# Optimization experiments

Hardware: AMD Instinct MI355X
Metric: run time of the kernel (lower is better)

The kernel has to match this reference:

```python
import jax, jax.numpy as jnp
import numpy as np

N, D, C, P = 4096, 512, 100, 64
EPS_COS = 1e-8   # torch cosine_similarity norm clamp
EPS_INV = 1e-5   # module's 1/(d + 1e-5)


def setup_inputs() -> dict:
    key = jax.random.key(0)
    k1, k2, k3, k4 = jax.random.split(key, 4)
    feats = jax.random.normal(k1, (N, D), dtype=jnp.float32)
    protos = jax.random.normal(k2, (C, P, D), dtype=jnp.float32)
    cls_ids = jax.random.randint(k3, (N,), 0, C)
    proto_labels = jax.random.randint(k4, (C, P), 0, 1000)
    return {"feats": feats, "protos": protos, "cls_ids": cls_ids,
            "proto_labels": proto_labels}


def reference(feats, protos, cls_ids, proto_labels):
    # Gather each box's class-conditional prototype set: [N, P, D]
    p = protos[cls_ids]
    pl = proto_labels[cls_ids]                       # [N, P]

    # cosine distance: 1 - f.p / (max(|f|,eps) * max(|p|,eps))
    dot = jnp.einsum('nd,npd->np', feats, p)         # [N, P]
    fnorm = jnp.maximum(jnp.linalg.norm(feats, axis=-1, keepdims=True), EPS_COS)
    pnorm = jnp.maximum(jnp.linalg.norm(p, axis=-1), EPS_COS)
    d_cos = 1.0 - dot / (fnorm * pnorm)

    diff = feats[:, None, :] - p                     # [N, P, D]
    d_l1 = jnp.mean(jnp.abs(diff), axis=-1)          # F.l1_loss (mean)
    d_l2 = jnp.mean(diff * diff, axis=-1)            # F.mse_loss (mean)

    dists = jnp.stack([d_cos, d_l1, d_l2], axis=1)   # [N, 3, P]
    probs = jax.nn.softmax(1.0 / (dists + EPS_INV), axis=-1).mean(axis=1)  # [N, P]

    idx = jnp.argmax(probs, axis=-1)                 # [N]
    labels = jnp.take_along_axis(pl, idx[:, None], axis=1)[:, 0]
    return labels, probs
```

## Files before the change

kernel.cpp:

```cpp
#include <hip/hip_runtime.h>

#define D 512
#define P 64
#define CHUNK 16
#define MAXD 1152
#define EPS_COS 1e-8f
#define EPS_INV 1e-5f


__device__ __forceinline__ float wave_sum(float v) {
#pragma unroll
    for (int m = 32; m >= 1; m >>= 1) v += __shfl_xor(v, m, 64);
    return v;
}

__global__ __launch_bounds__(256) void proto_norm_kernel(
    const float* __restrict__ protos, float* __restrict__ pp, int rows)
{
    const int lane = threadIdx.x & 63;
    const int r = blockIdx.x * 4 + (threadIdx.x >> 6);
    if (r >= rows) return;
    const float* row = protos + (size_t)r * D;
    const float4 a = *(const float4*)(row + lane * 4);
    const float4 b = *(const float4*)(row + 256 + lane * 4);
    float s = a.x*a.x + a.y*a.y + a.z*a.z + a.w*a.w
            + b.x*b.x + b.y*b.y + b.z*b.z + b.w*b.w;
    s = wave_sum(s);
    if (lane == 0) pp[r] = s;
}

__global__ __launch_bounds__(1024) void setup_kernel(
    const int* __restrict__ cls, int* __restrict__ sorted,
    int* __restrict__ desc, int N, int C)
{
    __shared__ int cnt[128], fl[128], exc[128], arr[128];
    const int t = threadIdx.x;
    if (t < 128) { cnt[t] = 0; fl[t] = 0; arr[t] = 0; }
    for (int i = t; i < 3 * MAXD; i += 1024) desc[i] = 0;
    __syncthreads();
#pragma unroll
    for (int k = 0; k < 4; ++k) {
        const int n = t + 1024 * k;
        if (n < N) atomicAdd(&cnt[cls[n]], 1);
    }
    __syncthreads();
    int v = 0, gv = 0, pos = 0;
    if (t < 128) {
        v = cnt[t];
        gv = (v + CHUNK - 1) / CHUNK;
        pos = ((t & 3) << 5) | (t >> 2);
        exc[t] = v;
        arr[pos] = gv;
    }
    __syncthreads();
    for (int d = 1; d < 128; d <<= 1) {
        int a = 0, b = 0;
        if (t < 128 && t >= d) { a = exc[t - d]; b = arr[t - d]; }
        __syncthreads();
        if (t < 128 && t >= d) { exc[t] += a; arr[t] += b; }
        __syncthreads();
    }
    int base = 0;
    if (t < 128) base = exc[t] - v;
    __syncthreads();
    if (t < 128) exc[t] = base;
    __syncthreads();
    if (t < C && gv > 0) {
        const int b = t & 3;
        const int bstart = (pos >= 32) ? arr[(pos & ~31) - 1] : 0;
        const int localoff = (arr[pos] - gv) - bstart;
        for (int k = 0; k < gv; ++k) {
            const int slot = ((localoff + k) << 2) | b;
            desc[3*slot+0] = t;
            desc[3*slot+1] = base + CHUNK * k;
            desc[3*slot+2] = min(CHUNK, v - CHUNK * k);
        }
    }
#pragma unroll
    for (int k = 0; k < 4; ++k) {
        const int n = t + 1024 * k;
        if (n < N) {
            const int c = cls[n];
            const int p2 = exc[c] + atomicAdd(&fl[c], 1);
            sorted[p2] = n;
        }
    }
}

__global__ __launch_bounds__(256, 3) void proto_dist_kernel(
    const float* __restrict__ feats,
    const float* __restrict__ protos,
    const int*   __restrict__ sorted,
    const int*   __restrict__ desc,
    float* __restrict__ dist)
{
    const int di   = blockIdx.x >> 1;
    const int half = blockIdx.x & 1;
    const int cnt  = desc[3*di+2];
    if (cnt == 0) return;
    const int cls   = desc[3*di+0];
    const int start = desc[3*di+1];
    const int lane = threadIdx.x & 63;
    const int wave = threadIdx.x >> 6;

    int  nidx[4];
    bool valid[4];
#pragma unroll
    for (int k = 0; k < 4; ++k) {
        const int pos = wave + 4 * k;
        valid[k] = pos < cnt;
        nidx[k]  = sorted[start + (valid[k] ? pos : (cnt - 1))];
    }

    float4 f0[4], f1[4];
#pragma unroll
    for (int b = 0; b < 4; ++b) {
        const float* f = feats + (size_t)nidx[b] * D;
        f0[b] = *(const float4*)(f + lane * 4);
        f1[b] = *(const float4*)(f + 256 + lane * 4);
    }

    const float* pr = protos + (size_t)cls * (P * D) + (size_t)half * (32 * D);
    const bool hi32 = (lane & 32) != 0;
    const bool hi16 = (lane & 16) != 0;
    const bool hi8  = (lane & 8)  != 0;

    float r_dot[4], r_l1[4];

    for (int g = 0; g < 4; ++g) {
        float pd[4][8], pl[4][8];
#pragma unroll
        for (int j = 0; j < 8; ++j) {
            const float* row = pr + (size_t)(8 * g + j) * D;
            const float4 q0 = *(const float4*)(row + lane * 4);
            const float4 q1 = *(const float4*)(row + 256 + lane * 4);
#pragma unroll
            for (int b = 0; b < 4; ++b) {
                float dot, l1, t;
                dot  = f0[b].x*q0.x; t = f0[b].x - q0.x; l1  = fabsf(t);
                dot += f0[b].y*q0.y; t = f0[b].y - q0.y; l1 += fabsf(t);
                dot += f0[b].z*q0.z; t = f0[b].z - q0.z; l1 += fabsf(t);
                dot += f0[b].w*q0.w; t = f0[b].w - q0.w; l1 += fabsf(t);
                dot += f1[b].x*q1.x; t = f1[b].x - q1.x; l1 += fabsf(t);
                dot += f1[b].y*q1.y; t = f1[b].y - q1.y; l1 += fabsf(t);
                dot += f1[b].z*q1.z; t = f1[b].z - q1.z; l1 += fabsf(t);
                dot += f1[b].w*q1.w; t = f1[b].w - q1.w; l1 += fabsf(t);
                pd[b][j] = dot; pl[b][j] = l1;
            }
        }
#pragma unroll
        for (int b = 0; b < 4; ++b) {
#pragma unroll
            for (int k = 0; k < 4; ++k) {
                const float sd = hi32 ? pd[b][k] : pd[b][k+4];
                const float sl = hi32 ? pl[b][k] : pl[b][k+4];
                const float rd = __shfl_xor(sd, 32, 64);
                const float rl = __shfl_xor(sl, 32, 64);
                pd[b][k] = (hi32 ? pd[b][k+4] : pd[b][k]) + rd;
                pl[b][k] = (hi32 ? pl[b][k+4] : pl[b][k]) + rl;
            }
#pragma unroll
            for (int k = 0; k < 2; ++k) {
                const float sd = hi16 ? pd[b][k] : pd[b][k+2];
                const float sl = hi16 ? pl[b][k] : pl[b][k+2];
                const float rd = __shfl_xor(sd, 16, 64);
                const float rl = __shfl_xor(sl, 16, 64);
                pd[b][k] = (hi16 ? pd[b][k+2] : pd[b][k]) + rd;
                pl[b][k] = (hi16 ? pl[b][k+2] : pl[b][k]) + rl;
            }
            {
                const float sd = hi8 ? pd[b][0] : pd[b][1];
                const float sl = hi8 ? pl[b][0] : pl[b][1];
                const float rd = __shfl_xor(sd, 8, 64);
                const float rl = __shfl_xor(sl, 8, 64);
                pd[b][0] = (hi8 ? pd[b][1] : pd[b][0]) + rd;
                pl[b][0] = (hi8 ? pl[b][1] : pl[b][0]) + rl;
            }
#pragma unroll
            for (int m = 4; m >= 1; m >>= 1) {
                pd[b][0] += __shfl_xor(pd[b][0], m, 64);
                pl[b][0] += __shfl_xor(pl[b][0], m, 64);
            }
            if ((lane & 3) == g) { r_dot[b] = pd[b][0]; r_l1[b] = pl[b][0]; }
        }
    }

    const int pg   = 32 * half + 8 * (lane & 3) + ((lane >> 3) & 7);
    const int qsel = (lane >> 2) & 1;
#pragma unroll
    for (int k = 0; k < 4; ++k) {
        if (valid[k]) {
            dist[((size_t)nidx[k] * P + pg) * 2 + qsel] = qsel ? r_l1[k] : r_dot[k];
        }
    }
}

__global__ __launch_bounds__(256) void softmax_kernel(
    const float* __restrict__ feats,
    const int*   __restrict__ cls_ids,
    const int*   __restrict__ proto_labels,
    const float* __restrict__ ppbuf,
    const float* __restrict__ dist,
    float* __restrict__ out, int N)
{
    const int lane = threadIdx.x & 63;
    const int n = blockIdx.x * 4 + (threadIdx.x >> 6);
    if (n >= N) return;
    const int cls = cls_ids[n];

    const float* f = feats + (size_t)n * D;
    const float4 a = *(const float4*)(f + lane * 4);
    const float4 b = *(const float4*)(f + 256 + lane * 4);
    float ffv = a.x*a.x + a.y*a.y + a.z*a.z + a.w*a.w
              + b.x*b.x + b.y*b.y + b.z*b.z + b.w*b.w;
    ffv = wave_sum(ffv);

    const float2 dl = *(const float2*)&dist[((size_t)n * P + lane) * 2];
    const float ppv   = ppbuf[cls * P + lane];
    const float fnorm = fmaxf(sqrtf(ffv), EPS_COS);
    const float pnorm = fmaxf(sqrtf(ppv), EPS_COS);
    const float d_cos = 1.0f - dl.x / (fnorm * pnorm);
    const float d_l1  = dl.y * (1.0f / (float)D);
    const float d_l2  = (ffv - 2.0f * dl.x + ppv) * (1.0f / (float)D);

    float sc[3];
    sc[0] = 1.0f / (d_cos + EPS_INV);
    sc[1] = 1.0f / (d_l1  + EPS_INV);
    sc[2] = 1.0f / (d_l2  + EPS_INV);

    float prob = 0.f;
#pragma unroll
    for (int i = 0; i < 3; ++i) {
        float m = sc[i];
#pragma unroll
        for (int w = 32; w >= 1; w >>= 1) m = fmaxf(m, __shfl_xor(m, w, 64));
        const float e = expf(sc[i] - m);
        prob += e / wave_sum(e);
    }
    prob *= (1.0f / 3.0f);

    float best = prob;
    int   bidx = lane;
#pragma unroll
    for (int w = 32; w >= 1; w >>= 1) {
        const float ov = __shfl_xor(best, w, 64);
        const int   oi = __shfl_xor(bidx, w, 64);
        if (ov > best || (ov == best && oi < bidx)) { best = ov; bidx = oi; }
    }

    out[(size_t)N + (size_t)n * P + lane] = prob;
    if (lane == 0) out[n] = (float)proto_labels[cls * P + bidx];
}

extern "C" void kernel_launch(void* const* d_in, const int* in_sizes, int n_in,
                              void* d_out, int out_size, void* d_ws, size_t ws_size,
                              hipStream_t stream) {
    const float* feats        = (const float*)d_in[0];
    const float* protos       = (const float*)d_in[1];
    const int*   cls_ids      = (const int*)d_in[2];
    const int*   proto_labels = (const int*)d_in[3];
    float* out = (float*)d_out;

    const int N    = in_sizes[2];
    const int rows = in_sizes[1] / D;
    const int C    = rows / P;

    char* w = (char*)d_ws;
    float* pp     = (float*)w;
    int*   sorted = (int*)(w + 25600);
    int*   desc   = (int*)(w + 41984);
    float* dist   = (float*)(w + 57344);

    proto_norm_kernel<<<(rows + 3) / 4, 256, 0, stream>>>(protos, pp, rows);
    setup_kernel<<<1, 1024, 0, stream>>>(cls_ids, sorted, desc, N, C);
    proto_dist_kernel<<<2 * MAXD, 256, 0, stream>>>(feats, protos, sorted, desc, dist);
    softmax_kernel<<<(N + 3) / 4, 256, 0, stream>>>(
        feats, cls_ids, proto_labels, pp, dist, out, N);
}
```

Baseline: 119.8 us.

## Fuse softmax into distance kernel and merge prep kernels into one launch

Merges the prototype-norm and class-sorting setup into one prep kernel, where block 0 does the sort and the other blocks compute norms. The distance and softmax stages become one kernel that handles all 64 prototypes per block for chunks of 4 features, computes feature norms inline, and writes probabilities and labels directly. This removes two launches and the intermediate distance buffer round trip through global memory. In exchange, each prototype set is re-read for fewer features, so L2 traffic on prototypes grows. Descriptor slots are now bounds-checked against the enlarged table.

```diff
diff --git a/kernel.cpp b/kernel.cpp
--- a/kernel.cpp
+++ b/kernel.cpp
@@ -2,8 +2,8 @@
 
 #define D 512
 #define P 64
-#define CHUNK 16
-#define MAXD 1152
+#define CHUNK 4
+#define MAXD 1536
 #define EPS_COS 1e-8f
 #define EPS_INV 1e-5f
 
@@ -14,33 +14,33 @@
     return v;
 }
 
-__global__ __launch_bounds__(256) void proto_norm_kernel(
-    const float* __restrict__ protos, float* __restrict__ pp, int rows)
+__global__ __launch_bounds__(256) void prep_kernel(
+    const float* __restrict__ protos, const int* __restrict__ cls,
+    float* __restrict__ pp, int* __restrict__ sorted, int* __restrict__ desc,
+    int N, int C, int rows)
 {
-    const int lane = threadIdx.x & 63;
-    const int r = blockIdx.x * 4 + (threadIdx.x >> 6);
-    if (r >= rows) return;
-    const float* row = protos + (size_t)r * D;
-    const float4 a = *(const float4*)(row + lane * 4);
-    const float4 b = *(const float4*)(row + 256 + lane * 4);
-    float s = a.x*a.x + a.y*a.y + a.z*a.z + a.w*a.w
-            + b.x*b.x + b.y*b.y + b.z*b.z + b.w*b.w;
-    s = wave_sum(s);
-    if (lane == 0) pp[r] = s;
-}
-
-__global__ __launch_bounds__(1024) void setup_kernel(
-    const int* __restrict__ cls, int* __restrict__ sorted,
-    int* __restrict__ desc, int N, int C)
-{
+    if (blockIdx.x != 0) {
+        const int lane = threadIdx.x & 63;
+        const int r = (blockIdx.x - 1) * 4 + (threadIdx.x >> 6);
+        if (r >= rows) return;
+        const float* row = protos + (size_t)r * D;
+        const float4 a = *(const float4*)(row + lane * 4);
+        const float4 b = *(const float4*)(row + 256 + lane * 4);
+        float s = a.x*a.x + a.y*a.y + a.z*a.z + a.w*a.w
+                + b.x*b.x + b.y*b.y + b.z*b.z + b.w*b.w;
+        s = wave_sum(s);
+        if (lane == 0) pp[r] = s;
+        return;
+    }
+
     __shared__ int cnt[128], fl[128], exc[128], arr[128];
     const int t = threadIdx.x;
     if (t < 128) { cnt[t] = 0; fl[t] = 0; arr[t] = 0; }
-    for (int i = t; i < 3 * MAXD; i += 1024) desc[i] = 0;
-    __syncthreads();
-#pragma unroll
-    for (int k = 0; k < 4; ++k) {
-        const int n = t + 1024 * k;
+    for (int i = t; i < 3 * MAXD; i += 256) desc[i] = 0;
+    __syncthreads();
+#pragma unroll
+    for (int k = 0; k < 16; ++k) {
+        const int n = t + 256 * k;
         if (n < N) atomicAdd(&cnt[cls[n]], 1);
     }
     __syncthreads();
@@ -48,7 +48,7 @@
     if (t < 128) {
         v = cnt[t];
         gv = (v + CHUNK - 1) / CHUNK;
-        pos = ((t & 3) << 5) | (t >> 2);
+        pos = ((t & 7) << 4) | (t >> 3);
         exc[t] = v;
         arr[pos] = gv;
     }
@@ -60,25 +60,26 @@
         if (t < 128 && t >= d) { exc[t] += a; arr[t] += b; }
         __syncthreads();
     }
-    int base = 0;
-    if (t < 128) base = exc[t] - v;
+    const int base = (t < 128) ? exc[t] - v : 0;
     __syncthreads();
     if (t < 128) exc[t] = base;
     __syncthreads();
     if (t < C && gv > 0) {
-        const int b = t & 3;
-        const int bstart = (pos >= 32) ? arr[(pos & ~31) - 1] : 0;
+        const int bucket = t & 7;
+        const int bstart = bucket ? arr[(bucket << 4) - 1] : 0;
         const int localoff = (arr[pos] - gv) - bstart;
         for (int k = 0; k < gv; ++k) {
-            const int slot = ((localoff + k) << 2) | b;
-            desc[3*slot+0] = t;
-            desc[3*slot+1] = base + CHUNK * k;
-            desc[3*slot+2] = min(CHUNK, v - CHUNK * k);
-        }
-    }
-#pragma unroll
-    for (int k = 0; k < 4; ++k) {
-        const int n = t + 1024 * k;
+            const int slot = ((localoff + k) << 3) | bucket;
+            if (slot < MAXD) {
+                desc[3*slot+0] = t;
+                desc[3*slot+1] = base + CHUNK * k;
+                desc[3*slot+2] = min(CHUNK, v - CHUNK * k);
+            }
+        }
+    }
+#pragma unroll
+    for (int k = 0; k < 16; ++k) {
+        const int n = t + 256 * k;
         if (n < N) {
             const int c = cls[n];
             const int p2 = exc[c] + atomicAdd(&fl[c], 1);
@@ -87,55 +88,62 @@
     }
 }
 
-__global__ __launch_bounds__(256, 3) void proto_dist_kernel(
+__global__ __launch_bounds__(128) void proto_main_kernel(
     const float* __restrict__ feats,
     const float* __restrict__ protos,
+    const int*   __restrict__ proto_labels,
+    const float* __restrict__ ppbuf,
     const int*   __restrict__ sorted,
     const int*   __restrict__ desc,
-    float* __restrict__ dist)
+    float* __restrict__ out, int N)
 {
-    const int di   = blockIdx.x >> 1;
-    const int half = blockIdx.x & 1;
-    const int cnt  = desc[3*di+2];
+    const int di  = blockIdx.x;
+    const int cnt = desc[3*di+2];
     if (cnt == 0) return;
     const int cls   = desc[3*di+0];
     const int start = desc[3*di+1];
     const int lane = threadIdx.x & 63;
     const int wave = threadIdx.x >> 6;
 
-    int  nidx[4];
-    bool valid[4];
-#pragma unroll
-    for (int k = 0; k < 4; ++k) {
-        const int pos = wave + 4 * k;
+    int  nidx[2];
+    bool valid[2];
+#pragma unroll
+    for (int k = 0; k < 2; ++k) {
+        const int pos = wave + 2 * k;
         valid[k] = pos < cnt;
         nidx[k]  = sorted[start + (valid[k] ? pos : (cnt - 1))];
     }
 
-    float4 f0[4], f1[4];
-#pragma unroll
-    for (int b = 0; b < 4; ++b) {
+    float4 f0[2], f1[2];
+    float  ff[2];
+#pragma unroll
+    for (int b = 0; b < 2; ++b) {
         const float* f = feats + (size_t)nidx[b] * D;
         f0[b] = *(const float4*)(f + lane * 4);
         f1[b] = *(const float4*)(f + 256 + lane * 4);
-    }
-
-    const float* pr = protos + (size_t)cls * (P * D) + (size_t)half * (32 * D);
+        float s = f0[b].x*f0[b].x + f0[b].y*f0[b].y + f0[b].z*f0[b].z + f0[b].w*f0[b].w
+                + f1[b].x*f1[b].x + f1[b].y*f1[b].y + f1[b].z*f1[b].z + f1[b].w*f1[b].w;
+        ff[b] = wave_sum(s);
+    }
+
+    const float* pr = protos + (size_t)cls * (P * D);
+    const int jsel = (lane >> 3) & 7;
+    const int gown = lane & 7;
     const bool hi32 = (lane & 32) != 0;
     const bool hi16 = (lane & 16) != 0;
     const bool hi8  = (lane & 8)  != 0;
 
-    float r_dot[4], r_l1[4];
-
-    for (int g = 0; g < 4; ++g) {
-        float pd[4][8], pl[4][8];
+    float r_dot[2] = {0.f, 0.f}, r_l1[2] = {0.f, 0.f};
+
+    for (int g = 0; g < 8; ++g) {
+        float pd[2][8], pl[2][8];
 #pragma unroll
         for (int j = 0; j < 8; ++j) {
             const float* row = pr + (size_t)(8 * g + j) * D;
             const float4 q0 = *(const float4*)(row + lane * 4);
             const float4 q1 = *(const float4*)(row + 256 + lane * 4);
 #pragma unroll
-            for (int b = 0; b < 4; ++b) {
+            for (int b = 0; b < 2; ++b) {
                 float dot, l1, t;
                 dot  = f0[b].x*q0.x; t = f0[b].x - q0.x; l1  = fabsf(t);
                 dot += f0[b].y*q0.y; t = f0[b].y - q0.y; l1 += fabsf(t);
@@ -149,7 +157,7 @@
             }
         }
 #pragma unroll
-        for (int b = 0; b < 4; ++b) {
+        for (int b = 0; b < 2; ++b) {
 #pragma unroll
             for (int k = 0; k < 4; ++k) {
                 const float sd = hi32 ? pd[b][k] : pd[b][k+4];
@@ -181,75 +189,51 @@
                 pd[b][0] += __shfl_xor(pd[b][0], m, 64);
                 pl[b][0] += __shfl_xor(pl[b][0], m, 64);
             }
-            if ((lane & 3) == g) { r_dot[b] = pd[b][0]; r_l1[b] = pl[b][0]; }
-        }
-    }
-
-    const int pg   = 32 * half + 8 * (lane & 3) + ((lane >> 3) & 7);
-    const int qsel = (lane >> 2) & 1;
-#pragma unroll
-    for (int k = 0; k < 4; ++k) {
-        if (valid[k]) {
-            dist[((size_t)nidx[k] * P + pg) * 2 + qsel] = qsel ? r_l1[k] : r_dot[k];
-        }
-    }
-}
-
-__global__ __launch_bounds__(256) void softmax_kernel(
-    const float* __restrict__ feats,
-    const int*   __restrict__ cls_ids,
-    const int*   __restrict__ proto_labels,
-    const float* __restrict__ ppbuf,
-    const float* __restrict__ dist,
-    float* __restrict__ out, int N)
-{
-    const int lane = threadIdx.x & 63;
-    const int n = blockIdx.x * 4 + (threadIdx.x >> 6);
-    if (n >= N) return;
-    const int cls = cls_ids[n];
-
-    const float* f = feats + (size_t)n * D;
-    const float4 a = *(const float4*)(f + lane * 4);
-    const float4 b = *(const float4*)(f + 256 + lane * 4);
-    float ffv = a.x*a.x + a.y*a.y + a.z*a.z + a.w*a.w
-              + b.x*b.x + b.y*b.y + b.z*b.z + b.w*b.w;
-    ffv = wave_sum(ffv);
-
-    const float2 dl = *(const float2*)&dist[((size_t)n * P + lane) * 2];
-    const float ppv   = ppbuf[cls * P + lane];
-    const float fnorm = fmaxf(sqrtf(ffv), EPS_COS);
-    const float pnorm = fmaxf(sqrtf(ppv), EPS_COS);
-    const float d_cos = 1.0f - dl.x / (fnorm * pnorm);
-    const float d_l1  = dl.y * (1.0f / (float)D);
-    const float d_l2  = (ffv - 2.0f * dl.x + ppv) * (1.0f / (float)D);
-
-    float sc[3];
-    sc[0] = 1.0f / (d_cos + EPS_INV);
-    sc[1] = 1.0f / (d_l1  + EPS_INV);
-    sc[2] = 1.0f / (d_l2  + EPS_INV);
-
-    float prob = 0.f;
-#pragma unroll
-    for (int i = 0; i < 3; ++i) {
-        float m = sc[i];
-#pragma unroll
-        for (int w = 32; w >= 1; w >>= 1) m = fmaxf(m, __shfl_xor(m, w, 64));
-        const float e = expf(sc[i] - m);
-        prob += e / wave_sum(e);
-    }
-    prob *= (1.0f / 3.0f);
-
-    float best = prob;
-    int   bidx = lane;
-#pragma unroll
-    for (int w = 32; w >= 1; w >>= 1) {
-        const float ov = __shfl_xor(best, w, 64);
-        const int   oi = __shfl_xor(bidx, w, 64);
-        if (ov > best || (ov == best && oi < bidx)) { best = ov; bidx = oi; }
-    }
-
-    out[(size_t)N + (size_t)n * P + lane] = prob;
-    if (lane == 0) out[n] = (float)proto_labels[cls * P + bidx];
+            if (gown == g) { r_dot[b] = pd[b][0]; r_l1[b] = pl[b][0]; }
+        }
+    }
+
+    const int myp = 8 * gown + jsel;
+    const float s_pp  = ppbuf[cls * P + myp];
+    const float pnorm = fmaxf(sqrtf(s_pp), EPS_COS);
+
+#pragma unroll
+    for (int b = 0; b < 2; ++b) {
+        const float fnorm = fmaxf(sqrtf(ff[b]), EPS_COS);
+        const float d_cos = 1.0f - r_dot[b] / (fnorm * pnorm);
+        const float d_l1  = r_l1[b] * (1.0f / (float)D);
+        const float d_l2  = (ff[b] - 2.0f * r_dot[b] + s_pp) * (1.0f / (float)D);
+
+        float sc[3];
+        sc[0] = 1.0f / (d_cos + EPS_INV);
+        sc[1] = 1.0f / (d_l1  + EPS_INV);
+        sc[2] = 1.0f / (d_l2  + EPS_INV);
+
+        float prob = 0.f;
+#pragma unroll
+        for (int i = 0; i < 3; ++i) {
+            float m = sc[i];
+#pragma unroll
+            for (int w = 32; w >= 1; w >>= 1) m = fmaxf(m, __shfl_xor(m, w, 64));
+            const float e = expf(sc[i] - m);
+            prob += e / wave_sum(e);
+        }
+        prob *= (1.0f / 3.0f);
+
+        float best = prob;
+        int   bidx = myp;
+#pragma unroll
+        for (int w = 32; w >= 1; w >>= 1) {
+            const float ov = __shfl_xor(best, w, 64);
+            const int   oi = __shfl_xor(bidx, w, 64);
+            if (ov > best || (ov == best && oi < bidx)) { best = ov; bidx = oi; }
+        }
+
+        if (valid[b]) {
+            out[(size_t)N + (size_t)nidx[b] * P + myp] = prob;
+            if (lane == 0) out[nidx[b]] = (float)proto_labels[cls * P + bidx];
+        }
+    }
 }
 
 extern "C" void kernel_launch(void* const* d_in, const int* in_sizes, int n_in,
@@ -269,11 +253,9 @@
     float* pp     = (float*)w;
     int*   sorted = (int*)(w + 25600);
     int*   desc   = (int*)(w + 41984);
-    float* dist   = (float*)(w + 57344);
-
-    proto_norm_kernel<<<(rows + 3) / 4, 256, 0, stream>>>(protos, pp, rows);
-    setup_kernel<<<1, 1024, 0, stream>>>(cls_ids, sorted, desc, N, C);
-    proto_dist_kernel<<<2 * MAXD, 256, 0, stream>>>(feats, protos, sorted, desc, dist);
-    softmax_kernel<<<(N + 3) / 4, 256, 0, stream>>>(
-        feats, cls_ids, proto_labels, pp, dist, out, N);
-}
+
+    prep_kernel<<<1 + (rows + 3) / 4, 256, 0, stream>>>(
+        protos, cls_ids, pp, sorted, desc, N, C, rows);
+    proto_main_kernel<<<MAXD, 128, 0, stream>>>(
+        feats, protos, proto_labels, pp, sorted, desc, out, N);
+}
```

Result: faster. 114.2 us (-4.7%).
